# Kernel optimization log

Hardware: AMD Instinct MI355X
Metric: run time of the kernel (lower is better)

The kernel has to match this reference:

```python
import jax, jax.numpy as jnp
import numpy as np

D_MODEL = 1024
N_HEADS = 16
D_HEAD = D_MODEL // N_HEADS  # 64
D_FF = D_MODEL  # FeedForward(d_model, d_model) in source
B, S = 4, 1024
EPS = 1e-5


def layer_norm(x, gamma, beta):
    mu = jnp.mean(x, axis=-1, keepdims=True)
    var = jnp.mean(jnp.square(x - mu), axis=-1, keepdims=True)
    return (x - mu) * jax.lax.rsqrt(var + EPS) * gamma + beta


def setup_inputs() -> dict:
    key = jax.random.key(0)
    ks = jax.random.split(key, 16)
    s_embed = 1.0 / np.sqrt(D_MODEL)
    s_ff = 1.0 / np.sqrt(D_FF)
    return {
        "x": jax.random.normal(ks[0], (B, S, D_MODEL), jnp.float32),
        # per-head QKV projections stacked over heads: [H, d_embed, d_head]
        "Wq": jax.random.normal(ks[1], (N_HEADS, D_MODEL, D_HEAD), jnp.float32) * s_embed,
        "bq": jax.random.normal(ks[2], (N_HEADS, D_HEAD), jnp.float32) * s_embed,
        "Wk": jax.random.normal(ks[3], (N_HEADS, D_MODEL, D_HEAD), jnp.float32) * s_embed,
        "bk": jax.random.normal(ks[4], (N_HEADS, D_HEAD), jnp.float32) * s_embed,
        "Wv": jax.random.normal(ks[5], (N_HEADS, D_MODEL, D_HEAD), jnp.float32) * s_embed,
        "bv": jax.random.normal(ks[6], (N_HEADS, D_HEAD), jnp.float32) * s_embed,
        "Wo": jax.random.normal(ks[7], (D_MODEL, D_MODEL), jnp.float32) * s_embed,
        "bo": jax.random.normal(ks[8], (D_MODEL,), jnp.float32) * s_embed,
        "g1": jnp.ones((D_MODEL,), jnp.float32),
        "be1": jnp.zeros((D_MODEL,), jnp.float32),
        "W1": jax.random.normal(ks[9], (D_MODEL, D_FF), jnp.float32) * s_embed,
        "b1": jax.random.normal(ks[10], (D_FF,), jnp.float32) * s_embed,
        "W2": jax.random.normal(ks[11], (D_FF, D_MODEL), jnp.float32) * s_ff,
        "b2": jax.random.normal(ks[12], (D_MODEL,), jnp.float32) * s_ff,
        "g2": jnp.ones((D_MODEL,), jnp.float32),
        "be2": jnp.zeros((D_MODEL,), jnp.float32),
    }


def reference(x, Wq, bq, Wk, bk, Wv, bv, Wo, bo, g1, be1, W1, b1, W2, b2, g2, be2):
    scale = 1.0 / np.sqrt(D_HEAD).astype(np.float32)
    # batched per-head projections (equivalent to the per-head Linear loop)
    Q = jnp.einsum('bse,hed->bhsd', x, Wq) + bq[None, :, None, :]
    K = jnp.einsum('bse,hed->bhsd', x, Wk) + bk[None, :, None, :]
    V = jnp.einsum('bse,hed->bhsd', x, Wv) + bv[None, :, None, :]
    scores = jnp.einsum('bhsd,bhtd->bhst', Q, K) * scale
    attn = jax.nn.softmax(scores, axis=-1)
    ctx = jnp.einsum('bhst,bhtd->bhsd', attn, V)
    # concat heads along feature dim (head order matches the torch cat)
    ctx = jnp.transpose(ctx, (0, 2, 1, 3)).reshape(x.shape[0], x.shape[1], D_MODEL)
    attn_out = ctx @ Wo + bo
    y1 = layer_norm(x + attn_out, g1, be1)
    ff = jax.nn.relu(y1 @ W1 + b1) @ W2 + b2  # dropout is identity in eval
    return layer_norm(y1 + ff, g2, be2)
```

## Files before the change

### kernel.cpp

```cpp
#include <hip/hip_runtime.h>
#include <stdint.h>

#define BSZ 4
#define SEQ 1024
#define DM 1024
#define NH 16
#define DH 64
#define ROWS (BSZ * SEQ)
#define QS3 3072

typedef unsigned short u16;
typedef short bf16x8 __attribute__((ext_vector_type(8)));
typedef float f32x4 __attribute__((ext_vector_type(4)));

__device__ __forceinline__ float b2f(u16 u) {
    union { uint32_t i; float f; } v; v.i = ((uint32_t)u) << 16; return v.f;
}
__device__ __forceinline__ u16 f2b(float f) {
    union { float f; uint32_t i; } v; v.f = f;
    uint32_t u = v.i;
    return (u16)((u + 0x7FFFu + ((u >> 16) & 1u)) >> 16);
}
__device__ __forceinline__ u16 f2b_rh(float f) {
    union { float f; uint32_t i; } v; v.f = f;
    return (u16)((v.i + 0x8000u) >> 16);
}

__device__ __forceinline__ size_t blk_idx(int row, int col, int nkt) {
    return (((size_t)((row >> 7) * nkt + (col >> 5))) << 12)
         + ((((row >> 4) & 7) * 64 + ((col >> 3) & 3) * 16 + (row & 15)) << 3)
         + (col & 7);
}

typedef const __attribute__((address_space(1))) void gv_t;
typedef __attribute__((address_space(3))) void lv_t;
__device__ __forceinline__ void gl_lds16(const void* g, void* l) {
    __builtin_amdgcn_global_load_lds((gv_t*)g, (lv_t*)l, 16, 0, 0);
}

__global__ __launch_bounds__(256) void detect_dtype(
    const uint32_t* __restrict__ x, int* __restrict__ flag)
{
    __shared__ int red[256];
    const int tid = threadIdx.x;
    int sane = 0;
    for (int i = tid; i < 1024; i += 256) {
        uint32_t w = x[i];
        uint32_t lo = w & 0xFFFFu;
        uint32_t e = (lo >> 7) & 0xFF;
        if ((e >= 100 && e <= 140) || lo == 0) sane++;
    }
    red[tid] = sane;
    __syncthreads();
    for (int st = 128; st > 0; st >>= 1) {
        if (tid < st) red[tid] += red[tid + st];
        __syncthreads();
    }
    if (tid == 0) flag[0] = (red[0] < 512) ? 1 : 0;
}

__global__ __launch_bounds__(256) void prep_all(
    const void* x_raw, const void* Wq, const void* Wk, const void* Wv,
    const void* Wo, const void* W1, const void* W2,
    const void* bq, const void* bk, const void* bv, const void* bo,
    const void* b1, const void* b2, const void* g1, const void* be1,
    const void* g2, const void* be2,
    u16* __restrict__ x_b, u16* __restrict__ WqkvB, u16* __restrict__ WoB,
    u16* __restrict__ W1B, u16* __restrict__ W2B, u16* __restrict__ vecs,
    const int* __restrict__ flag)
{
    const int bid = blockIdx.x, tid = threadIdx.x;
    const int isf = flag[0];

    if (bid < 2048) {
        const int gid = bid * 256 + tid;
        const int tile = gid >> 9, c = gid & 511;
        const int p = tile >> 5, t = tile & 31;
        const int r = p * 128 + ((c >> 6) & 7) * 16 + (c & 15);
        const int k = t * 32 + ((c >> 4) & 3) * 8;
        union { uint4 q; u16 s[8]; } o;
        if (isf) {
            const float* s = (const float*)x_raw + (size_t)r * DM + k;
            float4 f0 = *(const float4*)s;
            float4 f1 = *(const float4*)(s + 4);
            o.s[0] = f2b(f0.x); o.s[1] = f2b(f0.y); o.s[2] = f2b(f0.z); o.s[3] = f2b(f0.w);
            o.s[4] = f2b(f1.x); o.s[5] = f2b(f1.y); o.s[6] = f2b(f1.z); o.s[7] = f2b(f1.w);
        } else {
            o.q = *(const uint4*)((const u16*)x_raw + (size_t)r * DM + k);
        }
        *(uint4*)&x_b[(size_t)gid * 8] = o.q;
        return;
    }
    if (bid >= 8192) {
        const int i = (bid - 8192) * 256 + tid;
        const int seg = i >> 10, off = i & 1023;
        const void* srcs[10] = {bq, bk, bv, bo, b1, b2, g1, be1, g2, be2};
        const void* s = srcs[seg];
        vecs[i] = isf ? f2b(((const float*)s)[off]) : ((const u16*)s)[off];
        return;
    }

    const void* src; u16* dst; int R, C, n_off, bx, by, z;
    if (bid < 5120) {
        const int which = (bid - 2048) >> 10;
        const int lb = (bid - 2048) & 1023;
        src = which == 0 ? Wq : (which == 1 ? Wk : Wv);
        dst = WqkvB; R = DM; C = DH; n_off = which * 1024;
        bx = lb & 1; by = (lb >> 1) & 31; z = lb >> 6;
    } else {
        const int which = (bid - 5120) >> 10;
        const int lb = (bid - 5120) & 1023;
        src = which == 0 ? Wo : (which == 1 ? W1 : W2);
        dst = which == 0 ? WoB : (which == 1 ? W1B : W2B);
        R = DM; C = DM; n_off = 0;
        bx = lb & 31; by = (lb >> 5) & 31; z = 0;
    }

    __shared__ u16 Ts[32][33];
    const int cb = bx * 32, rb = by * 32;
    const int tr = tid >> 3, tc4 = (tid & 7) * 4;
    const size_t sbase = (size_t)z * R * C;

    u16 v[4];
    if (isf) {
        const float* s = (const float*)src + sbase + (size_t)(rb + tr) * C + cb + tc4;
        float4 f = *(const float4*)s;
        v[0] = f2b(f.x); v[1] = f2b(f.y); v[2] = f2b(f.z); v[3] = f2b(f.w);
    } else {
        const u16* s = (const u16*)src + sbase + (size_t)(rb + tr) * C + cb + tc4;
        ushort4 f = *(const ushort4*)s;
        v[0] = f.x; v[1] = f.y; v[2] = f.z; v[3] = f.w;
    }
    #pragma unroll
    for (int j = 0; j < 4; ++j) Ts[tc4 + j][tr] = v[j];
    __syncthreads();

    if (tid < 128) {
        const int np = tid & 31, qp = tid >> 5;
        const int n = n_off + z * C + cb + np;
        const int k = rb + qp * 8;
        union { uint4 q; u16 s[8]; } o;
        #pragma unroll
        for (int j = 0; j < 8; ++j) o.s[j] = Ts[np][qp * 8 + j];
        *(uint4*)&dst[blk_idx(n, k, 32)] = o.q;
    }
}

__global__ __launch_bounds__(256) void gemm_qkv(
    const u16* __restrict__ Ab, const u16* __restrict__ Bb,
    const u16* __restrict__ bias,
    u16* __restrict__ Qblk, u16* __restrict__ Kblk, u16* __restrict__ Vblk)
{
    __shared__ uint4 smem4[2176];
    u16* As = (u16*)smem4;
    u16* Bs = (u16*)smem4 + 8192;
    u16* Cs = (u16*)smem4;

    const int tid = threadIdx.x;
    const int w = tid >> 6, lane = tid & 63;
    const int l16 = lane & 15, quad = lane >> 4;
    const int wr = w >> 1, wc = w & 1;
    const int bm = blockIdx.y * 128, bn = blockIdx.x * 128;
    const int nkt = 32;

    const u16* At = Ab + ((size_t)(bm >> 7) * nkt << 12);
    const u16* Bt = Bb + ((size_t)(bn >> 7) * nkt << 12);

    f32x4 acc[4][4];
    #pragma unroll
    for (int i = 0; i < 4; ++i)
        #pragma unroll
        for (int j = 0; j < 4; ++j)
            acc[i][j] = (f32x4){0.f, 0.f, 0.f, 0.f};

    const int co0 = (w * 64) * 8, co1 = (256 + w * 64) * 8;

    gl_lds16(&At[(w * 64 + lane) * 8],         &As[co0]);
    gl_lds16(&At[(256 + w * 64 + lane) * 8],   &As[co1]);
    gl_lds16(&Bt[(w * 64 + lane) * 8],         &Bs[co0]);
    gl_lds16(&Bt[(256 + w * 64 + lane) * 8],   &Bs[co1]);
    __syncthreads();

    for (int kt = 0; kt < nkt; ++kt) {
        const int cur = (kt & 1) * 4096, nxt = cur ^ 4096;
        if (kt + 1 < nkt) {
            const size_t tb = (size_t)(kt + 1) << 12;
            gl_lds16(&At[tb + (w * 64 + lane) * 8],       &As[nxt + co0]);
            gl_lds16(&At[tb + (256 + w * 64 + lane) * 8], &As[nxt + co1]);
            gl_lds16(&Bt[tb + (w * 64 + lane) * 8],       &Bs[nxt + co0]);
            gl_lds16(&Bt[tb + (256 + w * 64 + lane) * 8], &Bs[nxt + co1]);
        }

        bf16x8 a[4], b[4];
        #pragma unroll
        for (int i = 0; i < 4; ++i)
            a[i] = *(const bf16x8*)&As[cur + (((wr * 4 + i) * 64) + quad * 16 + l16) * 8];
        #pragma unroll
        for (int j = 0; j < 4; ++j)
            b[j] = *(const bf16x8*)&Bs[cur + (((wc * 4 + j) * 64) + quad * 16 + l16) * 8];

        #pragma unroll
        for (int i = 0; i < 4; ++i)
            #pragma unroll
            for (int j = 0; j < 4; ++j)
                acc[i][j] = __builtin_amdgcn_mfma_f32_16x16x32_bf16(a[i], b[j], acc[i][j], 0, 0, 0);
        __syncthreads();
    }

    #pragma unroll
    for (int j = 0; j < 4; ++j) {
        const int lc = wc * 64 + j * 16 + l16;
        const float bj = b2f(bias[bn + lc]);
        #pragma unroll
        for (int i = 0; i < 4; ++i)
            #pragma unroll
            for (int r = 0; r < 4; ++r) {
                const int lr = wr * 64 + i * 16 + quad * 4 + r;
                Cs[lr * 136 + lc] = f2b(acc[i][j][r] + bj);
            }
    }
    __syncthreads();

    const int b_ = bm >> 10, sb16 = (bm & 1023) >> 4, kb64 = (bm & 1023) >> 6;
    if (bn < 2048) {
        u16* out = (bn < 1024) ? Qblk : Kblk;
        const int hbase = (bn & 1023) >> 6;
        #pragma unroll
        for (int u = 0; u < 8; ++u) {
            const int g = u * 256 + tid;
            const int hh = g >> 10, rem = g & 1023;
            const int s16r = rem >> 7, rem2 = rem & 127;
            const int half = rem2 >> 6, lam = rem2 & 63;
            const int row = s16r * 16 + (lam & 15);
            const int col = hh * 64 + half * 32 + (lam >> 4) * 8;
            uint4 val = *(const uint4*)&Cs[row * 136 + col];
            const size_t gi = ((size_t)((b_ * 16 + hbase + hh) * 64 + sb16 + s16r)) * 1024
                            + half * 512 + (size_t)lam * 8;
            *(uint4*)&out[gi] = val;
        }
    } else {
        const int hbase = (bn - 2048) >> 6;
        #pragma unroll
        for (int u = 0; u < 8; ++u) {
            const int g = u * 256 + tid;
            const int hh = g >> 10, rem = g & 1023;
            const int kt64r = rem >> 9, dt = (rem >> 7) & 3;
            const int half = (rem >> 6) & 1, lam = rem & 63;
            const int d = dt * 16 + (lam & 15);
            const int s0 = kt64r * 64 + half * 32 + (lam >> 4) * 8;
            union { uint4 q; u16 s[8]; } o;
            #pragma unroll
            for (int j = 0; j < 8; ++j) o.s[j] = Cs[(s0 + j) * 136 + hh * 64 + d];
            const size_t gi = ((size_t)((b_ * 16 + hbase + hh) * 16 + kb64 + kt64r)) * 4096
                            + dt * 1024 + half * 512 + (size_t)lam * 8;
            *(uint4*)&Vblk[gi] = o.q;
        }
    }
}

__global__ __launch_bounds__(256) void gemm_b64(
    const u16* __restrict__ Ab, const u16* __restrict__ Bb,
    const u16* __restrict__ bias, const u16* __restrict__ resid,
    u16* __restrict__ C, int M, int N, int K,
    int relu, int c_blocked, int resid_blocked)
{
    __shared__ uint4 smem4[1536];
    u16* As = (u16*)smem4;
    u16* Bs = (u16*)smem4 + 8192;
    u16* Cs = (u16*)smem4;

    const int tid = threadIdx.x;
    const int w = tid >> 6, lane = tid & 63;
    const int l16 = lane & 15, quad = lane >> 4;
    const int bm = blockIdx.y * 128, bn = blockIdx.x * 64;
    const int nkt = K >> 5;

    const u16* At = Ab + ((size_t)(bm >> 7) * nkt << 12);
    const int bsub = ((bn >> 6) & 1) * 256;
    const u16* Bt = Bb + ((size_t)(bn >> 7) * nkt << 12);

    f32x4 acc[2][4];
    #pragma unroll
    for (int i = 0; i < 2; ++i)
        #pragma unroll
        for (int j = 0; j < 4; ++j)
            acc[i][j] = (f32x4){0.f, 0.f, 0.f, 0.f};

    const int co0 = (w * 64) * 8, co1 = (256 + w * 64) * 8;

    gl_lds16(&At[(w * 64 + lane) * 8],        &As[co0]);
    gl_lds16(&At[(256 + w * 64 + lane) * 8],  &As[co1]);
    gl_lds16(&Bt[(bsub + w * 64 + lane) * 8], &Bs[co0]);
    __syncthreads();

    for (int kt = 0; kt < nkt; ++kt) {
        const int curA = (kt & 1) * 4096, nxtA = curA ^ 4096;
        const int curB = (kt & 1) * 2048, nxtB = curB ^ 2048;
        if (kt + 1 < nkt) {
            const size_t tb = (size_t)(kt + 1) << 12;
            gl_lds16(&At[tb + (w * 64 + lane) * 8],        &As[nxtA + co0]);
            gl_lds16(&At[tb + (256 + w * 64 + lane) * 8],  &As[nxtA + co1]);
            gl_lds16(&Bt[tb + (bsub + w * 64 + lane) * 8], &Bs[nxtB + co0]);
        }

        bf16x8 a[2], b[4];
        #pragma unroll
        for (int i = 0; i < 2; ++i)
            a[i] = *(const bf16x8*)&As[curA + (((w * 2 + i) * 64) + quad * 16 + l16) * 8];
        #pragma unroll
        for (int j = 0; j < 4; ++j)
            b[j] = *(const bf16x8*)&Bs[curB + ((j * 64) + quad * 16 + l16) * 8];

        #pragma unroll
        for (int i = 0; i < 2; ++i)
            #pragma unroll
            for (int j = 0; j < 4; ++j)
                acc[i][j] = __builtin_amdgcn_mfma_f32_16x16x32_bf16(a[i], b[j], acc[i][j], 0, 0, 0);
        __syncthreads();
    }

    #pragma unroll
    for (int j = 0; j < 4; ++j) {
        const int lc = j * 16 + l16;
        const int col = bn + lc;
        const float bj = bias ? b2f(bias[col]) : 0.f;
        #pragma unroll
        for (int i = 0; i < 2; ++i) {
            #pragma unroll
            for (int r = 0; r < 4; ++r) {
                const int lr = w * 32 + i * 16 + quad * 4 + r;
                float v = acc[i][j][r] + bj;
                if (resid) {
                    const size_t ri = resid_blocked ? blk_idx(bm + lr, col, N >> 5)
                                                    : (size_t)(bm + lr) * N + col;
                    v += b2f(resid[ri]);
                }
                if (relu) v = v > 0.f ? v : 0.f;
                Cs[lr * 72 + lc] = f2b(v);
            }
        }
    }
    __syncthreads();

    if (!c_blocked) {
        #pragma unroll
        for (int u = 0; u < 4; ++u) {
            const int g = u * 256 + tid;
            const int row = g >> 3, c16 = g & 7;
            uint4 val = *(const uint4*)&Cs[row * 72 + c16 * 8];
            *(uint4*)&C[(size_t)(bm + row) * N + bn + c16 * 8] = val;
        }
    } else {
        const size_t obase = ((size_t)((bm >> 7) * (N >> 5) + (bn >> 5))) << 12;
        #pragma unroll
        for (int u = 0; u < 4; ++u) {
            const int cc = u * 256 + tid;
            const int t2 = cc >> 9, c = cc & 511;
            const int row = ((c >> 6) & 7) * 16 + (c & 15);
            const int col = t2 * 32 + ((c >> 4) & 3) * 8;
            uint4 val = *(const uint4*)&Cs[row * 72 + col];
            *(uint4*)&C[obase + ((size_t)t2 << 12) + (size_t)c * 8] = val;
        }
    }
}

__global__ __launch_bounds__(512) void attn_mfma(
    const u16* __restrict__ Qblk, const u16* __restrict__ Kblk,
    const u16* __restrict__ Vblk, u16* __restrict__ ctx)
{
    __shared__ u16 Qf[8192];
    __shared__ u16 Kf[2][4096];
    __shared__ u16 Vf[2][4096];
    __shared__ u16 Ps[8 * 16 * 72];

    const int qt = blockIdx.x, h = blockIdx.y, b = blockIdx.z;
    const int tid = threadIdx.x;
    const int w = tid >> 6, lane = tid & 63;
    const int l16 = lane & 15, quad = lane >> 4;
    const size_t qrow0 = (size_t)(b * SEQ + qt * 128);
    const int bh = b * NH + h;
    const int hoff = h * DH;

    const u16* Qg = Qblk + ((size_t)(bh * 64 + qt * 8 + w)) * 1024 + (size_t)lane * 8;
    gl_lds16(Qg,       &Qf[w * 1024]);
    gl_lds16(Qg + 512, &Qf[w * 1024 + 512]);

    const u16* Kg = Kblk + ((size_t)(bh * 64)) * 1024 + (size_t)w * 512 + (size_t)lane * 8;
    const u16* Vg = Vblk + ((size_t)(bh * 16)) * 4096 + (size_t)w * 512 + (size_t)lane * 8;

    gl_lds16(Kg, &Kf[0][w * 512]);
    gl_lds16(Vg, &Vf[0][w * 512]);
    __syncthreads();

    bf16x8 aQ0 = *(const bf16x8*)&Qf[w * 1024 +       lane * 8];
    bf16x8 aQ1 = *(const bf16x8*)&Qf[w * 1024 + 512 + lane * 8];

    f32x4 O[4];
    #pragma unroll
    for (int dt = 0; dt < 4; ++dt) O[dt] = (f32x4){0.f, 0.f, 0.f, 0.f};
    float lacc[4] = {0.f, 0.f, 0.f, 0.f};

    for (int kt64 = 0; kt64 < SEQ / 64; ++kt64) {
        const int cur = kt64 & 1, nxt = cur ^ 1;
        if (kt64 + 1 < SEQ / 64) {
            gl_lds16(Kg + (size_t)(kt64 + 1) * 4096, &Kf[nxt][w * 512]);
            gl_lds16(Vg + (size_t)(kt64 + 1) * 4096, &Vf[nxt][w * 512]);
        }

        f32x4 St[4];
        #pragma unroll
        for (int t = 0; t < 4; ++t) {
            bf16x8 b0 = *(const bf16x8*)&Kf[cur][t * 1024 +       lane * 8];
            bf16x8 b1 = *(const bf16x8*)&Kf[cur][t * 1024 + 512 + lane * 8];
            f32x4 z = (f32x4){0.f, 0.f, 0.f, 0.f};
            z = __builtin_amdgcn_mfma_f32_16x16x32_bf16(aQ0, b0, z, 0, 0, 0);
            z = __builtin_amdgcn_mfma_f32_16x16x32_bf16(aQ1, b1, z, 0, 0, 0);
            St[t] = z;
        }

        #pragma unroll
        for (int t = 0; t < 4; ++t)
            #pragma unroll
            for (int r = 0; r < 4; ++r) {
                const float p = __expf(St[t][r] * 0.125f);
                lacc[r] += p;
                Ps[w * 1152 + (quad * 4 + r) * 72 + t * 16 + l16] = f2b_rh(p);
            }

        bf16x8 aP0 = *(const bf16x8*)&Ps[w * 1152 + l16 * 72 +  0 + quad * 8];
        bf16x8 aP1 = *(const bf16x8*)&Ps[w * 1152 + l16 * 72 + 32 + quad * 8];
        #pragma unroll
        for (int dt = 0; dt < 4; ++dt) {
            bf16x8 vv0 = *(const bf16x8*)&Vf[cur][dt * 1024 +       lane * 8];
            bf16x8 vv1 = *(const bf16x8*)&Vf[cur][dt * 1024 + 512 + lane * 8];
            O[dt] = __builtin_amdgcn_mfma_f32_16x16x32_bf16(aP0, vv0, O[dt], 0, 0, 0);
            O[dt] = __builtin_amdgcn_mfma_f32_16x16x32_bf16(aP1, vv1, O[dt], 0, 0, 0);
        }
        __syncthreads();
    }

    const size_t pbase = ((size_t)(qrow0 >> 7) * 32) << 12;
    #pragma unroll
    for (int r = 0; r < 4; ++r) {
        float s = lacc[r];
        s += __shfl_xor(s, 1);
        s += __shfl_xor(s, 2);
        s += __shfl_xor(s, 4);
        s += __shfl_xor(s, 8);
        const float inv = 1.0f / s;
        #pragma unroll
        for (int dt = 0; dt < 4; ++dt) {
            const int t = (hoff + dt * 16) >> 5;
            const int q = (((hoff + dt * 16) >> 3) & 3);
            const size_t idx = pbase + ((size_t)t << 12)
                             + ((w * 64 + q * 16 + quad * 4 + r) << 3) + (l16 & 7);
            const size_t idx2 = idx + (((size_t)(l16 >> 3)) << 7);
            ctx[idx2] = f2b(O[dt][r] * inv);
        }
    }
}

__global__ __launch_bounds__(256) void layernorm_kernel(
    const u16* __restrict__ X, const u16* __restrict__ gamma,
    const u16* __restrict__ beta, void* __restrict__ Y,
    const int* __restrict__ flag, int y_mode)
{
    __shared__ float red[256], red2[256];
    const int r = blockIdx.x, tid = threadIdx.x;
    const u16* xp = X + (size_t)r * DM;

    ushort4 v = *(const ushort4*)(xp + tid * 4);
    float x0 = b2f(v.x), x1 = b2f(v.y), x2 = b2f(v.z), x3 = b2f(v.w);
    red[tid]  = x0 + x1 + x2 + x3;
    red2[tid] = x0 * x0 + x1 * x1 + x2 * x2 + x3 * x3;
    __syncthreads();
    for (int st = 128; st > 0; st >>= 1) {
        if (tid < st) { red[tid] += red[tid + st]; red2[tid] += red2[tid + st]; }
        __syncthreads();
    }
    const float mu = red[0] * (1.0f / DM);
    const float var = red2[0] * (1.0f / DM) - mu * mu;
    const float rstd = rsqrtf(var + 1e-5f);

    ushort4 g = *(const ushort4*)(gamma + tid * 4);
    ushort4 be = *(const ushort4*)(beta + tid * 4);
    float y0 = (x0 - mu) * rstd * b2f(g.x) + b2f(be.x);
    float y1 = (x1 - mu) * rstd * b2f(g.y) + b2f(be.y);
    float y2 = (x2 - mu) * rstd * b2f(g.z) + b2f(be.z);
    float y3 = (x3 - mu) * rstd * b2f(g.w) + b2f(be.w);

    const int k = tid * 4;
    if (y_mode == 2 && flag[0]) {
        float* yp = (float*)Y + (size_t)r * DM + k;
        yp[0] = y0; yp[1] = y1; yp[2] = y2; yp[3] = y3;
    } else if (y_mode == 1) {
        u16* yp = (u16*)Y + blk_idx(r, k, 32);
        ushort4 o; o.x = f2b(y0); o.y = f2b(y1); o.z = f2b(y2); o.w = f2b(y3);
        *(ushort4*)yp = o;
    } else {
        u16* yp = (u16*)Y + (size_t)r * DM + k;
        ushort4 o; o.x = f2b(y0); o.y = f2b(y1); o.z = f2b(y2); o.w = f2b(y3);
        *(ushort4*)yp = o;
    }
}

extern "C" void kernel_launch(void* const* d_in, const int* in_sizes, int n_in,
                              void* d_out, int out_size, void* d_ws, size_t ws_size,
                              hipStream_t stream) {
    const void* x_raw   = d_in[0];
    const void* Wq_raw  = d_in[1];
    const void* bq_raw  = d_in[2];
    const void* Wk_raw  = d_in[3];
    const void* bk_raw  = d_in[4];
    const void* Wv_raw  = d_in[5];
    const void* bv_raw  = d_in[6];
    const void* Wo_raw  = d_in[7];
    const void* bo_raw  = d_in[8];
    const void* g1_raw  = d_in[9];
    const void* be1_raw = d_in[10];
    const void* W1_raw  = d_in[11];
    const void* b1_raw  = d_in[12];
    const void* W2_raw  = d_in[13];
    const void* b2_raw  = d_in[14];
    const void* g2_raw  = d_in[15];
    const void* be2_raw = d_in[16];

    char* ws = (char*)d_ws;
    const size_t MB = 1024 * 1024;
    int* flag   = (int*)ws;
    u16* x_b    = (u16*)(ws + 1 * MB);
    u16* WqkvB  = (u16*)(ws + 9 * MB);
    u16* WoB    = (u16*)(ws + 15 * MB);
    u16* W1B    = (u16*)(ws + 17 * MB);
    u16* W2B    = (u16*)(ws + 19 * MB);
    u16* vecs   = (u16*)(ws + 21 * MB);
    u16* bqkv_c = vecs;
    u16* bo_c   = vecs + 3072;
    u16* b1_c   = vecs + 4096;
    u16* b2_c   = vecs + 5120;
    u16* g1_c   = vecs + 6144;
    u16* be1_c  = vecs + 7168;
    u16* g2_c   = vecs + 8192;
    u16* be2_c  = vecs + 9216;
    u16* Qblk   = (u16*)(ws + 22 * MB);
    u16* Kblk   = (u16*)(ws + 30 * MB);
    u16* Vblk   = (u16*)(ws + 38 * MB);
    u16* ctxB   = (u16*)(ws + 48 * MB);
    u16* res1   = (u16*)(ws + 56 * MB);
    u16* y1B    = Qblk;
    u16* hmidB  = Kblk;
    u16* res2   = res1;

    detect_dtype<<<1, 256, 0, stream>>>((const uint32_t*)x_raw, flag);

    prep_all<<<8232, 256, 0, stream>>>(
        x_raw, Wq_raw, Wk_raw, Wv_raw, Wo_raw, W1_raw, W2_raw,
        bq_raw, bk_raw, bv_raw, bo_raw, b1_raw, b2_raw,
        g1_raw, be1_raw, g2_raw, be2_raw,
        x_b, WqkvB, WoB, W1B, W2B, vecs, flag);

    gemm_qkv<<<dim3(QS3 / 128, ROWS / 128), 256, 0, stream>>>(
        x_b, WqkvB, bqkv_c, Qblk, Kblk, Vblk);

    attn_mfma<<<dim3(SEQ / 128, NH, BSZ), 512, 0, stream>>>(Qblk, Kblk, Vblk, ctxB);

    dim3 gg64(DM / 64, ROWS / 128);
    gemm_b64<<<gg64, 256, 0, stream>>>(ctxB, WoB, bo_c, x_b, res1, ROWS, DM, DM, 0, 0, 1);
    layernorm_kernel<<<ROWS, 256, 0, stream>>>(res1, g1_c, be1_c, (void*)y1B, flag, 1);
    gemm_b64<<<gg64, 256, 0, stream>>>(y1B, W1B, b1_c, nullptr, hmidB, ROWS, DM, DM, 1, 1, 0);
    gemm_b64<<<gg64, 256, 0, stream>>>(hmidB, W2B, b2_c, y1B, res2, ROWS, DM, DM, 0, 0, 1);
    layernorm_kernel<<<ROWS, 256, 0, stream>>>(res2, g2_c, be2_c, d_out, flag, 2);
}
```

Measured before the change: 265.1 us.

## Fuse tail GEMMs and layernorms into one persistent kernel with panel counters

Replaces the five tail launches (Wo GEMM, LN1, FFN1, FFN2, LN2) with one 512-block kernel. Each block computes a 128x64 tile, then signals per-row-panel atomic counters in global memory, so dependent stages start as soon as their 128-row panel is ready instead of waiting for a whole-grid kernel boundary. Layernorm is rewritten as wave-per-row with shuffle reductions, eight rows per block. This relies on all 512 blocks being co-resident (launch bounds 256,2), since spin-waiting blocks could otherwise deadlock. The counters are zeroed in the detect kernel on every call.

```diff
diff --git a/kernel.cpp b/kernel.cpp
--- a/kernel.cpp
+++ b/kernel.cpp
@@ -38,11 +38,28 @@
     __builtin_amdgcn_global_load_lds((gv_t*)g, (lv_t*)l, 16, 0, 0);
 }
 
+__device__ __forceinline__ void panel_arrive(int* cnt) {
+    __syncthreads();
+    if (threadIdx.x == 0) {
+        __threadfence();
+        atomicAdd(cnt, 1);
+    }
+}
+__device__ __forceinline__ void panel_wait16(const int* cnt) {
+    if (threadIdx.x == 0) {
+        while (__hip_atomic_load(cnt, __ATOMIC_RELAXED, __HIP_MEMORY_SCOPE_AGENT) < 16)
+            __builtin_amdgcn_s_sleep(1);
+        __threadfence();
+    }
+    __syncthreads();
+}
+
 __global__ __launch_bounds__(256) void detect_dtype(
-    const uint32_t* __restrict__ x, int* __restrict__ flag)
+    const uint32_t* __restrict__ x, int* __restrict__ flag, int* __restrict__ cnts)
 {
     __shared__ int red[256];
     const int tid = threadIdx.x;
+    for (int i = tid; i < 2048; i += 256) cnts[i] = 0;
     int sane = 0;
     for (int i = tid; i < 1024; i += 256) {
         uint32_t w = x[i];
@@ -258,11 +275,107 @@
     }
 }
 
-__global__ __launch_bounds__(256) void gemm_b64(
+__global__ __launch_bounds__(512) void attn_mfma(
+    const u16* __restrict__ Qblk, const u16* __restrict__ Kblk,
+    const u16* __restrict__ Vblk, u16* __restrict__ ctx)
+{
+    __shared__ u16 Qf[8192];
+    __shared__ u16 Kf[2][4096];
+    __shared__ u16 Vf[2][4096];
+    __shared__ u16 Ps[8 * 16 * 72];
+
+    const int qt = blockIdx.x, h = blockIdx.y, b = blockIdx.z;
+    const int tid = threadIdx.x;
+    const int w = tid >> 6, lane = tid & 63;
+    const int l16 = lane & 15, quad = lane >> 4;
+    const size_t qrow0 = (size_t)(b * SEQ + qt * 128);
+    const int bh = b * NH + h;
+    const int hoff = h * DH;
+
+    const u16* Qg = Qblk + ((size_t)(bh * 64 + qt * 8 + w)) * 1024 + (size_t)lane * 8;
+    gl_lds16(Qg,       &Qf[w * 1024]);
+    gl_lds16(Qg + 512, &Qf[w * 1024 + 512]);
+
+    const u16* Kg = Kblk + ((size_t)(bh * 64)) * 1024 + (size_t)w * 512 + (size_t)lane * 8;
+    const u16* Vg = Vblk + ((size_t)(bh * 16)) * 4096 + (size_t)w * 512 + (size_t)lane * 8;
+
+    gl_lds16(Kg, &Kf[0][w * 512]);
+    gl_lds16(Vg, &Vf[0][w * 512]);
+    __syncthreads();
+
+    bf16x8 aQ0 = *(const bf16x8*)&Qf[w * 1024 +       lane * 8];
+    bf16x8 aQ1 = *(const bf16x8*)&Qf[w * 1024 + 512 + lane * 8];
+
+    f32x4 O[4];
+    #pragma unroll
+    for (int dt = 0; dt < 4; ++dt) O[dt] = (f32x4){0.f, 0.f, 0.f, 0.f};
+    float lacc[4] = {0.f, 0.f, 0.f, 0.f};
+
+    for (int kt64 = 0; kt64 < SEQ / 64; ++kt64) {
+        const int cur = kt64 & 1, nxt = cur ^ 1;
+        if (kt64 + 1 < SEQ / 64) {
+            gl_lds16(Kg + (size_t)(kt64 + 1) * 4096, &Kf[nxt][w * 512]);
+            gl_lds16(Vg + (size_t)(kt64 + 1) * 4096, &Vf[nxt][w * 512]);
+        }
+
+        f32x4 St[4];
+        #pragma unroll
+        for (int t = 0; t < 4; ++t) {
+            bf16x8 b0 = *(const bf16x8*)&Kf[cur][t * 1024 +       lane * 8];
+            bf16x8 b1 = *(const bf16x8*)&Kf[cur][t * 1024 + 512 + lane * 8];
+            f32x4 z = (f32x4){0.f, 0.f, 0.f, 0.f};
+            z = __builtin_amdgcn_mfma_f32_16x16x32_bf16(aQ0, b0, z, 0, 0, 0);
+            z = __builtin_amdgcn_mfma_f32_16x16x32_bf16(aQ1, b1, z, 0, 0, 0);
+            St[t] = z;
+        }
+
+        #pragma unroll
+        for (int t = 0; t < 4; ++t)
+            #pragma unroll
+            for (int r = 0; r < 4; ++r) {
+                const float p = __expf(St[t][r] * 0.125f);
+                lacc[r] += p;
+                Ps[w * 1152 + (quad * 4 + r) * 72 + t * 16 + l16] = f2b_rh(p);
+            }
+
+        bf16x8 aP0 = *(const bf16x8*)&Ps[w * 1152 + l16 * 72 +  0 + quad * 8];
+        bf16x8 aP1 = *(const bf16x8*)&Ps[w * 1152 + l16 * 72 + 32 + quad * 8];
+        #pragma unroll
+        for (int dt = 0; dt < 4; ++dt) {
+            bf16x8 vv0 = *(const bf16x8*)&Vf[cur][dt * 1024 +       lane * 8];
+            bf16x8 vv1 = *(const bf16x8*)&Vf[cur][dt * 1024 + 512 + lane * 8];
+            O[dt] = __builtin_amdgcn_mfma_f32_16x16x32_bf16(aP0, vv0, O[dt], 0, 0, 0);
+            O[dt] = __builtin_amdgcn_mfma_f32_16x16x32_bf16(aP1, vv1, O[dt], 0, 0, 0);
+        }
+        __syncthreads();
+    }
+
+    const size_t pbase = ((size_t)(qrow0 >> 7) * 32) << 12;
+    #pragma unroll
+    for (int r = 0; r < 4; ++r) {
+        float s = lacc[r];
+        s += __shfl_xor(s, 1);
+        s += __shfl_xor(s, 2);
+        s += __shfl_xor(s, 4);
+        s += __shfl_xor(s, 8);
+        const float inv = 1.0f / s;
+        #pragma unroll
+        for (int dt = 0; dt < 4; ++dt) {
+            const int t = (hoff + dt * 16) >> 5;
+            const int q = (((hoff + dt * 16) >> 3) & 3);
+            const size_t idx = pbase + ((size_t)t << 12)
+                             + ((w * 64 + q * 16 + quad * 4 + r) << 3) + (l16 & 7);
+            const size_t idx2 = idx + (((size_t)(l16 >> 3)) << 7);
+            ctx[idx2] = f2b(O[dt][r] * inv);
+        }
+    }
+}
+
+__device__ void gemm_tile(
     const u16* __restrict__ Ab, const u16* __restrict__ Bb,
     const u16* __restrict__ bias, const u16* __restrict__ resid,
-    u16* __restrict__ C, int M, int N, int K,
-    int relu, int c_blocked, int resid_blocked)
+    u16* __restrict__ C, int N, int K,
+    int relu, int c_blocked, int resid_blocked, int bx, int by)
 {
     __shared__ uint4 smem4[1536];
     u16* As = (u16*)smem4;
@@ -272,7 +385,7 @@
     const int tid = threadIdx.x;
     const int w = tid >> 6, lane = tid & 63;
     const int l16 = lane & 15, quad = lane >> 4;
-    const int bm = blockIdx.y * 128, bn = blockIdx.x * 64;
+    const int bm = by * 128, bn = bx * 64;
     const int nkt = K >> 5;
 
     const u16* At = Ab + ((size_t)(bm >> 7) * nkt << 12);
@@ -362,146 +475,120 @@
             *(uint4*)&C[obase + ((size_t)t2 << 12) + (size_t)c * 8] = val;
         }
     }
-}
-
-__global__ __launch_bounds__(512) void attn_mfma(
-    const u16* __restrict__ Qblk, const u16* __restrict__ Kblk,
-    const u16* __restrict__ Vblk, u16* __restrict__ ctx)
+    __syncthreads();
+}
+
+__device__ void ln8(
+    const u16* __restrict__ X, const u16* __restrict__ gamma,
+    const u16* __restrict__ beta, void* __restrict__ Y,
+    int y_mode, int isf, int row0)
 {
-    __shared__ u16 Qf[8192];
-    __shared__ u16 Kf[2][4096];
-    __shared__ u16 Vf[2][4096];
-    __shared__ u16 Ps[8 * 16 * 72];
-
-    const int qt = blockIdx.x, h = blockIdx.y, b = blockIdx.z;
     const int tid = threadIdx.x;
     const int w = tid >> 6, lane = tid & 63;
-    const int l16 = lane & 15, quad = lane >> 4;
-    const size_t qrow0 = (size_t)(b * SEQ + qt * 128);
-    const int bh = b * NH + h;
-    const int hoff = h * DH;
-
-    const u16* Qg = Qblk + ((size_t)(bh * 64 + qt * 8 + w)) * 1024 + (size_t)lane * 8;
-    gl_lds16(Qg,       &Qf[w * 1024]);
-    gl_lds16(Qg + 512, &Qf[w * 1024 + 512]);
-
-    const u16* Kg = Kblk + ((size_t)(bh * 64)) * 1024 + (size_t)w * 512 + (size_t)lane * 8;
-    const u16* Vg = Vblk + ((size_t)(bh * 16)) * 4096 + (size_t)w * 512 + (size_t)lane * 8;
-
-    gl_lds16(Kg, &Kf[0][w * 512]);
-    gl_lds16(Vg, &Vf[0][w * 512]);
-    __syncthreads();
-
-    bf16x8 aQ0 = *(const bf16x8*)&Qf[w * 1024 +       lane * 8];
-    bf16x8 aQ1 = *(const bf16x8*)&Qf[w * 1024 + 512 + lane * 8];
-
-    f32x4 O[4];
-    #pragma unroll
-    for (int dt = 0; dt < 4; ++dt) O[dt] = (f32x4){0.f, 0.f, 0.f, 0.f};
-    float lacc[4] = {0.f, 0.f, 0.f, 0.f};
-
-    for (int kt64 = 0; kt64 < SEQ / 64; ++kt64) {
-        const int cur = kt64 & 1, nxt = cur ^ 1;
-        if (kt64 + 1 < SEQ / 64) {
-            gl_lds16(Kg + (size_t)(kt64 + 1) * 4096, &Kf[nxt][w * 512]);
-            gl_lds16(Vg + (size_t)(kt64 + 1) * 4096, &Vf[nxt][w * 512]);
-        }
-
-        f32x4 St[4];
-        #pragma unroll
-        for (int t = 0; t < 4; ++t) {
-            bf16x8 b0 = *(const bf16x8*)&Kf[cur][t * 1024 +       lane * 8];
-            bf16x8 b1 = *(const bf16x8*)&Kf[cur][t * 1024 + 512 + lane * 8];
-            f32x4 z = (f32x4){0.f, 0.f, 0.f, 0.f};
-            z = __builtin_amdgcn_mfma_f32_16x16x32_bf16(aQ0, b0, z, 0, 0, 0);
-            z = __builtin_amdgcn_mfma_f32_16x16x32_bf16(aQ1, b1, z, 0, 0, 0);
-            St[t] = z;
-        }
-
-        #pragma unroll
-        for (int t = 0; t < 4; ++t)
+    union U8 { uint4 q; u16 h[8]; };
+
+    U8 ga, gb, ba, bb;
+    ga.q = *(const uint4*)(gamma + lane * 16);
+    gb.q = *(const uint4*)(gamma + lane * 16 + 8);
+    ba.q = *(const uint4*)(beta  + lane * 16);
+    bb.q = *(const uint4*)(beta  + lane * 16 + 8);
+    float g[16], be[16];
+    #pragma unroll
+    for (int j = 0; j < 8; ++j) {
+        g[j] = b2f(ga.h[j]);  g[8 + j] = b2f(gb.h[j]);
+        be[j] = b2f(ba.h[j]); be[8 + j] = b2f(bb.h[j]);
+    }
+
+    #pragma unroll
+    for (int it = 0; it < 2; ++it) {
+        const int r = row0 + it * 4 + w;
+        const u16* xp = X + (size_t)r * DM + lane * 16;
+        U8 xa, xb;
+        xa.q = *(const uint4*)xp;
+        xb.q = *(const uint4*)(xp + 8);
+        float xv[16], s = 0.f, s2 = 0.f;
+        #pragma unroll
+        for (int j = 0; j < 8; ++j) { xv[j] = b2f(xa.h[j]); xv[8 + j] = b2f(xb.h[j]); }
+        #pragma unroll
+        for (int j = 0; j < 16; ++j) { s += xv[j]; s2 += xv[j] * xv[j]; }
+        #pragma unroll
+        for (int d = 1; d < 64; d <<= 1) {
+            s  += __shfl_xor(s, d);
+            s2 += __shfl_xor(s2, d);
+        }
+        const float mu = s * (1.0f / DM);
+        const float rstd = rsqrtf(s2 * (1.0f / DM) - mu * mu + 1e-5f);
+
+        float y[16];
+        #pragma unroll
+        for (int j = 0; j < 16; ++j) y[j] = (xv[j] - mu) * rstd * g[j] + be[j];
+
+        if (y_mode == 1) {
             #pragma unroll
-            for (int r = 0; r < 4; ++r) {
-                const float p = __expf(St[t][r] * 0.125f);
-                lacc[r] += p;
-                Ps[w * 1152 + (quad * 4 + r) * 72 + t * 16 + l16] = f2b_rh(p);
+            for (int c = 0; c < 2; ++c) {
+                U8 o;
+                #pragma unroll
+                for (int j = 0; j < 8; ++j) o.h[j] = f2b(y[c * 8 + j]);
+                *(uint4*)&((u16*)Y)[blk_idx(r, lane * 16 + c * 8, 32)] = o.q;
             }
-
-        bf16x8 aP0 = *(const bf16x8*)&Ps[w * 1152 + l16 * 72 +  0 + quad * 8];
-        bf16x8 aP1 = *(const bf16x8*)&Ps[w * 1152 + l16 * 72 + 32 + quad * 8];
-        #pragma unroll
-        for (int dt = 0; dt < 4; ++dt) {
-            bf16x8 vv0 = *(const bf16x8*)&Vf[cur][dt * 1024 +       lane * 8];
-            bf16x8 vv1 = *(const bf16x8*)&Vf[cur][dt * 1024 + 512 + lane * 8];
-            O[dt] = __builtin_amdgcn_mfma_f32_16x16x32_bf16(aP0, vv0, O[dt], 0, 0, 0);
-            O[dt] = __builtin_amdgcn_mfma_f32_16x16x32_bf16(aP1, vv1, O[dt], 0, 0, 0);
-        }
-        __syncthreads();
-    }
-
-    const size_t pbase = ((size_t)(qrow0 >> 7) * 32) << 12;
-    #pragma unroll
-    for (int r = 0; r < 4; ++r) {
-        float s = lacc[r];
-        s += __shfl_xor(s, 1);
-        s += __shfl_xor(s, 2);
-        s += __shfl_xor(s, 4);
-        s += __shfl_xor(s, 8);
-        const float inv = 1.0f / s;
-        #pragma unroll
-        for (int dt = 0; dt < 4; ++dt) {
-            const int t = (hoff + dt * 16) >> 5;
-            const int q = (((hoff + dt * 16) >> 3) & 3);
-            const size_t idx = pbase + ((size_t)t << 12)
-                             + ((w * 64 + q * 16 + quad * 4 + r) << 3) + (l16 & 7);
-            const size_t idx2 = idx + (((size_t)(l16 >> 3)) << 7);
-            ctx[idx2] = f2b(O[dt][r] * inv);
-        }
-    }
-}
-
-__global__ __launch_bounds__(256) void layernorm_kernel(
-    const u16* __restrict__ X, const u16* __restrict__ gamma,
-    const u16* __restrict__ beta, void* __restrict__ Y,
-    const int* __restrict__ flag, int y_mode)
+        } else {
+            if (isf) {
+                float* yp = (float*)Y + (size_t)r * DM + lane * 16;
+                #pragma unroll
+                for (int c = 0; c < 4; ++c) {
+                    float4 f; f.x = y[c*4]; f.y = y[c*4+1]; f.z = y[c*4+2]; f.w = y[c*4+3];
+                    *(float4*)(yp + c * 4) = f;
+                }
+            } else {
+                u16* yp = (u16*)Y + (size_t)r * DM + lane * 16;
+                #pragma unroll
+                for (int c = 0; c < 2; ++c) {
+                    U8 o;
+                    #pragma unroll
+                    for (int j = 0; j < 8; ++j) o.h[j] = f2b(y[c * 8 + j]);
+                    *(uint4*)(yp + c * 8) = o.q;
+                }
+            }
+        }
+    }
+}
+
+__global__ __launch_bounds__(256, 2) void tail_fused(
+    const u16* __restrict__ ctxB, const u16* __restrict__ WoB,
+    const u16* __restrict__ W1B, const u16* __restrict__ W2B,
+    const u16* __restrict__ bo_c, const u16* __restrict__ b1_c,
+    const u16* __restrict__ b2_c,
+    const u16* __restrict__ g1_c, const u16* __restrict__ be1_c,
+    const u16* __restrict__ g2_c, const u16* __restrict__ be2_c,
+    const u16* __restrict__ x_b,
+    u16* __restrict__ res1, u16* __restrict__ y1B, u16* __restrict__ hmidB,
+    void* __restrict__ out, const int* __restrict__ flag, int* __restrict__ cnts)
 {
-    __shared__ float red[256], red2[256];
-    const int r = blockIdx.x, tid = threadIdx.x;
-    const u16* xp = X + (size_t)r * DM;
-
-    ushort4 v = *(const ushort4*)(xp + tid * 4);
-    float x0 = b2f(v.x), x1 = b2f(v.y), x2 = b2f(v.z), x3 = b2f(v.w);
-    red[tid]  = x0 + x1 + x2 + x3;
-    red2[tid] = x0 * x0 + x1 * x1 + x2 * x2 + x3 * x3;
-    __syncthreads();
-    for (int st = 128; st > 0; st >>= 1) {
-        if (tid < st) { red[tid] += red[tid + st]; red2[tid] += red2[tid + st]; }
-        __syncthreads();
-    }
-    const float mu = red[0] * (1.0f / DM);
-    const float var = red2[0] * (1.0f / DM) - mu * mu;
-    const float rstd = rsqrtf(var + 1e-5f);
-
-    ushort4 g = *(const ushort4*)(gamma + tid * 4);
-    ushort4 be = *(const ushort4*)(beta + tid * 4);
-    float y0 = (x0 - mu) * rstd * b2f(g.x) + b2f(be.x);
-    float y1 = (x1 - mu) * rstd * b2f(g.y) + b2f(be.y);
-    float y2 = (x2 - mu) * rstd * b2f(g.z) + b2f(be.z);
-    float y3 = (x3 - mu) * rstd * b2f(g.w) + b2f(be.w);
-
-    const int k = tid * 4;
-    if (y_mode == 2 && flag[0]) {
-        float* yp = (float*)Y + (size_t)r * DM + k;
-        yp[0] = y0; yp[1] = y1; yp[2] = y2; yp[3] = y3;
-    } else if (y_mode == 1) {
-        u16* yp = (u16*)Y + blk_idx(r, k, 32);
-        ushort4 o; o.x = f2b(y0); o.y = f2b(y1); o.z = f2b(y2); o.w = f2b(y3);
-        *(ushort4*)yp = o;
-    } else {
-        u16* yp = (u16*)Y + (size_t)r * DM + k;
-        ushort4 o; o.x = f2b(y0); o.y = f2b(y1); o.z = f2b(y2); o.w = f2b(y3);
-        *(ushort4*)yp = o;
-    }
+    const int bid = blockIdx.x;
+    const int bx = bid & 15, by = bid >> 4;
+    int* c_res1 = cnts + (0 * 32 + by) * 16;
+    int* c_y1   = cnts + (1 * 32 + by) * 16;
+    int* c_hmid = cnts + (2 * 32 + by) * 16;
+    int* c_res2 = cnts + (3 * 32 + by) * 16;
+    u16* res2 = res1;
+
+    gemm_tile(ctxB, WoB, bo_c, x_b, res1, DM, DM, 0, 0, 1, bx, by);
+    panel_arrive(c_res1);
+
+    panel_wait16(c_res1);
+    ln8(res1, g1_c, be1_c, y1B, 1, 0, bid * 8);
+    panel_arrive(c_y1);
+
+    panel_wait16(c_y1);
+    gemm_tile(y1B, W1B, b1_c, nullptr, hmidB, DM, DM, 1, 1, 0, bx, by);
+    panel_arrive(c_hmid);
+
+    panel_wait16(c_hmid);
+    gemm_tile(hmidB, W2B, b2_c, y1B, res2, DM, DM, 0, 0, 1, bx, by);
+    panel_arrive(c_res2);
+
+    panel_wait16(c_res2);
+    ln8(res2, g2_c, be2_c, out, 2, flag[0], bid * 8);
 }
 
 extern "C" void kernel_launch(void* const* d_in, const int* in_sizes, int n_in,
@@ -528,6 +615,7 @@
     char* ws = (char*)d_ws;
     const size_t MB = 1024 * 1024;
     int* flag   = (int*)ws;
+    int* cnts   = (int*)(ws + 4096);
     u16* x_b    = (u16*)(ws + 1 * MB);
     u16* WqkvB  = (u16*)(ws + 9 * MB);
     u16* WoB    = (u16*)(ws + 15 * MB);
@@ -549,9 +637,8 @@
     u16* res1   = (u16*)(ws + 56 * MB);
     u16* y1B    = Qblk;
     u16* hmidB  = Kblk;
-    u16* res2   = res1;
-
-    detect_dtype<<<1, 256, 0, stream>>>((const uint32_t*)x_raw, flag);
+
+    detect_dtype<<<1, 256, 0, stream>>>((const uint32_t*)x_raw, flag, cnts);
 
     prep_all<<<8232, 256, 0, stream>>>(
         x_raw, Wq_raw, Wk_raw, Wv_raw, Wo_raw, W1_raw, W2_raw,
@@ -564,10 +651,8 @@
 
     attn_mfma<<<dim3(SEQ / 128, NH, BSZ), 512, 0, stream>>>(Qblk, Kblk, Vblk, ctxB);
 
-    dim3 gg64(DM / 64, ROWS / 128);
-    gemm_b64<<<gg64, 256, 0, stream>>>(ctxB, WoB, bo_c, x_b, res1, ROWS, DM, DM, 0, 0, 1);
-    layernorm_kernel<<<ROWS, 256, 0, stream>>>(res1, g1_c, be1_c, (void*)y1B, flag, 1);
-    gemm_b64<<<gg64, 256, 0, stream>>>(y1B, W1B, b1_c, nullptr, hmidB, ROWS, DM, DM, 1, 1, 0);
-    gemm_b64<<<gg64, 256, 0, stream>>>(hmidB, W2B, b2_c, y1B, res2, ROWS, DM, DM, 0, 0, 1);
-    layernorm_kernel<<<ROWS, 256, 0, stream>>>(res2, g2_c, be2_c, d_out, flag, 2);
-}
+    tail_fused<<<512, 256, 0, stream>>>(
+        ctxB, WoB, W1B, W2B, bo_c, b1_c, b2_c,
+        g1_c, be1_c, g2_c, be2_c, x_b,
+        res1, y1B, hmidB, d_out, flag, cnts);
+}
```

Measured after the change: 391.3 us. 47.6% more time.
